# Kernel optimization log

Measured on AMD Instinct MI355X. Metric: run time of the kernel, lower is better.

## Reference

```python
import jax, jax.numpy as jnp
import numpy as np
from functools import partial

B, C, COND, L_MEL, HOP, UP = 4, 32, 80, 2048, 8, 8
LAYERS, K, HID, KPK, EMB = 4, 3, 64, 3, 512
L_AUD = L_MEL * UP  # 16384


def conv1d(x, w, b=None, padding=0, dilation=1):
    # x: (B, Cin, L), w: (Cout, Cin, K) -- PyTorch Conv1d semantics
    out = jax.lax.conv_general_dilated(
        x, w, window_strides=(1,), padding=[(padding, padding)],
        rhs_dilation=(dilation,), dimension_numbers=('NCH', 'OIH', 'NCH'))
    if b is not None:
        out = out + b[None, :, None]
    return out


def conv_transpose1d(x, w, stride, pad):
    # PyTorch ConvTranspose1d, weight (Cin, Cout, K), no bias, output_padding=0
    k = w.shape[-1]
    w_eq = jnp.flip(w, -1).transpose(1, 0, 2)  # (Cout, Cin, K)
    lo = k - 1 - pad
    return jax.lax.conv_general_dilated(
        x, w_eq, window_strides=(1,), padding=[(lo, lo)],
        lhs_dilation=(stride,), dimension_numbers=('NCH', 'OIH', 'NCH'))


def lrelu(x, s):
    return jnp.where(x >= 0, x, s * x)


def kernel_predictor(cond, kp_in_w, kp_in_b, kp_res_w1, kp_res_b1,
                     kp_res_w2, kp_res_b2, kp_k_w, kp_k_b, kp_b_w, kp_b_b):
    # FastDiff/UnivNet KernelPredictor: input conv (k=5) + 3 residual blocks + heads
    h = lrelu(conv1d(cond, kp_in_w, kp_in_b, padding=2), 0.1)
    for i in range(3):  # fixed small structural loop
        r = lrelu(conv1d(h, kp_res_w1[i], kp_res_b1[i], padding=1), 0.1)
        r = lrelu(conv1d(r, kp_res_w2[i], kp_res_b2[i], padding=1), 0.1)
        h = h + r
    bsz, _, ln = cond.shape
    k = conv1d(h, kp_k_w, kp_k_b, padding=1)
    b = conv1d(h, kp_b_w, kp_b_b, padding=1)
    kernels = k.reshape(bsz, LAYERS, C, 2 * C, K, ln)
    bias = b.reshape(bsz, LAYERS, 2 * C, ln)
    return kernels, bias


def location_variable_convolution(x, kernel, bias, dilation, hop):
    # x: (B, Cin, L), kernel: (B, Cin, Cout, K, Lf), bias: (B, Cout, Lf)
    bsz, cin, ln = x.shape
    _, _, cout, ks, lf = kernel.shape
    pad = dilation * (ks - 1) // 2
    xp = jnp.pad(x, ((0, 0), (0, 0), (pad, pad)))
    # gather per-frame sliding windows: (Lf, hop, K)
    pos = (jnp.arange(lf) * hop)[:, None, None] \
        + jnp.arange(hop)[None, :, None] \
        + (jnp.arange(ks) * dilation)[None, None, :]
    xw = xp[:, :, pos]  # (B, Cin, Lf, hop, K)
    o = jnp.einsum('bilsk,biokl->bols', xw, kernel)  # (B, Cout, Lf, hop)
    o = o + bias[:, :, :, None]
    return o.reshape(bsz, cout, lf * hop)


def forward(x, audio_down, c, noise_embedding, fc_t_w, fc_t_b, up_w, conv_w,
            kp_in_w, kp_in_b, kp_res_w1, kp_res_b1, kp_res_w2, kp_res_b2,
            kp_k_w, kp_k_b, kp_b_w, kp_b_b):
    noise = (noise_embedding @ fc_t_w.T + fc_t_b)[:, :, None]  # (B, 80, 1)
    condition = c + noise
    kernels, bias = kernel_predictor(condition, kp_in_w, kp_in_b, kp_res_w1,
                                     kp_res_b1, kp_res_w2, kp_res_b2,
                                     kp_k_w, kp_k_b, kp_b_w, kp_b_b)
    h = lrelu(x, 0.2)
    h = conv_transpose1d(h, up_w, UP, UP // 2)  # (B, 32, 16384)
    for i in range(LAYERS):
        h = h + audio_down
        y = lrelu(h, 0.2)
        y = conv1d(y, conv_w[i], padding=3 ** i, dilation=3 ** i)
        y = lrelu(y, 0.2)
        y = location_variable_convolution(y, kernels[:, i], bias[:, i], 1, HOP)
        h = h + jax.nn.sigmoid(y[:, :C, :]) * jnp.tanh(y[:, C:, :])
    return h


def setup_inputs() -> dict:
    key = jax.random.key(0)
    ks = jax.random.split(key, 20)
    s = 0.02
    kch = LAYERS * C * (2 * C) * K  # 24576
    bch = LAYERS * 2 * C            # 256
    return {
        'x': jax.random.normal(ks[0], (B, C, L_MEL), jnp.float32),
        'audio_down': jax.random.normal(ks[1], (B, C, L_AUD), jnp.float32),
        'c': jax.random.normal(ks[2], (B, COND, L_MEL), jnp.float32),
        'noise_embedding': jax.random.normal(ks[3], (B, EMB), jnp.float32),
        'fc_t_w': jax.random.normal(ks[4], (COND, EMB), jnp.float32) * s,
        'fc_t_b': jnp.zeros((COND,), jnp.float32),
        'up_w': jax.random.normal(ks[5], (C, C, UP * 2), jnp.float32) * s,
        'conv_w': jax.random.normal(ks[6], (LAYERS, C, C, K), jnp.float32) * s,
        'kp_in_w': jax.random.normal(ks[7], (HID, COND, 5), jnp.float32) * s,
        'kp_in_b': jnp.zeros((HID,), jnp.float32),
        'kp_res_w1': jax.random.normal(ks[8], (3, HID, HID, KPK), jnp.float32) * s,
        'kp_res_b1': jnp.zeros((3, HID), jnp.float32),
        'kp_res_w2': jax.random.normal(ks[9], (3, HID, HID, KPK), jnp.float32) * s,
        'kp_res_b2': jnp.zeros((3, HID), jnp.float32),
        'kp_k_w': jax.random.normal(ks[10], (kch, HID, KPK), jnp.float32) * s,
        'kp_k_b': jnp.zeros((kch,), jnp.float32),
        'kp_b_w': jax.random.normal(ks[11], (bch, HID, KPK), jnp.float32) * s,
        'kp_b_b': jnp.zeros((bch,), jnp.float32),
    }


def reference(x, audio_down, c, noise_embedding, fc_t_w, fc_t_b, up_w, conv_w,
              kp_in_w, kp_in_b, kp_res_w1, kp_res_b1, kp_res_w2, kp_res_b2,
              kp_k_w, kp_k_b, kp_b_w, kp_b_b):
    return forward(x, audio_down, c, noise_embedding, fc_t_w, fc_t_b, up_w,
                   conv_w, kp_in_w, kp_in_b, kp_res_w1, kp_res_b1, kp_res_w2,
                   kp_res_b2, kp_k_w, kp_k_b, kp_b_w, kp_b_b)
```

## Files before the change

kernel.cpp:

```cpp
#include <hip/hip_runtime.h>
#include <math.h>

#define B_      4
#define C_      32
#define COND_   80
#define LMEL_   2048
#define HOP_    8
#define UP_     8
#define LAYERS_ 4
#define K_      3
#define HID_    64
#define KPK_    3
#define EMB_    512
#define LAUD_   (LMEL_*UP_)
#define KCH_    (LAYERS_*C_*2*C_*K_)
#define BCH_    (LAYERS_*2*C_)
#define Y2S     (LAUD_ + 8)

typedef short v8s __attribute__((ext_vector_type(8)));
typedef float v4f __attribute__((ext_vector_type(4)));

__device__ __forceinline__ float lrelu_(float v, float s) { return v >= 0.f ? v : s * v; }

__device__ __forceinline__ unsigned short f2bf(float f) {
  unsigned int x = __float_as_uint(f);
  unsigned int r = (x + 0x7FFFu + ((x >> 16) & 1u)) >> 16;
  return (unsigned short)r;
}

#define GLOAD16(GSRC, LDST)                                              \
  __builtin_amdgcn_global_load_lds(                                     \
      (const __attribute__((address_space(1))) unsigned int*)(GSRC),    \
      (__attribute__((address_space(3))) unsigned int*)(LDST), 16, 0, 0)

__global__ void k_mkWTs(const float* __restrict__ src, float* __restrict__ dst,
                        int S, int OC, int ICK) {
  int idx = blockIdx.x*256 + threadIdx.x;
  if (idx >= S*OC*ICK) return;
  int s = idx / (OC*ICK), rem = idx % (OC*ICK);
  int oc = rem / ICK, ick = rem % ICK;
  dst[s*OC*ICK + ick*OC + oc] = src[idx];
}

__global__ void k_noise_cond(const float* __restrict__ ne, const float* __restrict__ fw,
                             const float* __restrict__ fb, const float* __restrict__ c,
                             float* __restrict__ cond) {
  int b = blockIdx.x / COND_;
  int cc = blockIdx.x % COND_;
  __shared__ float red[256];
  float p = 0.f;
  for (int j = threadIdx.x; j < EMB_; j += 256)
    p += ne[b*EMB_ + j] * fw[cc*EMB_ + j];
  red[threadIdx.x] = p;
  __syncthreads();
  for (int s = 128; s > 0; s >>= 1) {
    if (threadIdx.x < s) red[threadIdx.x] += red[threadIdx.x + s];
    __syncthreads();
  }
  float noise = red[0] + fb[cc];
  const float* cp = c + (b*COND_ + cc)*LMEL_;
  float* op = cond + (b*COND_ + cc)*LMEL_;
  for (int l = threadIdx.x; l < LMEL_; l += 256) op[l] = cp[l] + noise;
}

__global__ __launch_bounds__(256) void k_kp_in(const float* __restrict__ cond, const float* __restrict__ wT,
                                               const float* __restrict__ bias, float* __restrict__ out) {
  const int T = 32;
  int b  = blockIdx.x / (LMEL_/T);
  int lb = (blockIdx.x % (LMEL_/T)) * T;
  __shared__ float sc[COND_][T + 4];
  for (int idx = threadIdx.x; idx < COND_*(T+4); idx += 256) {
    int cc = idx / (T+4), j = idx % (T+4);
    int l = lb + j - 2;
    sc[cc][j] = (l >= 0 && l < LMEL_) ? cond[(b*COND_ + cc)*LMEL_ + l] : 0.f;
  }
  __syncthreads();
  int ch = threadIdx.x & 63;
  int lq = threadIdx.x >> 6;
  float acc[8];
#pragma unroll
  for (int ii = 0; ii < 8; ii++) acc[ii] = bias[ch];
  for (int cc = 0; cc < COND_; cc++) {
    float r[12];
#pragma unroll
    for (int j = 0; j < 12; j++) r[j] = sc[cc][lq*8 + j];
#pragma unroll
    for (int k = 0; k < 5; k++) {
      float wv = wT[(cc*5 + k)*64 + ch];
#pragma unroll
      for (int ii = 0; ii < 8; ii++) acc[ii] = fmaf(wv, r[ii + k], acc[ii]);
    }
  }
  float* op = out + (b*HID_ + ch)*LMEL_ + lb + lq*8;
#pragma unroll
  for (int ii = 0; ii < 8; ii++) acc[ii] = lrelu_(acc[ii], 0.1f);
  *reinterpret_cast<float4*>(&op[0]) = make_float4(acc[0], acc[1], acc[2], acc[3]);
  *reinterpret_cast<float4*>(&op[4]) = make_float4(acc[4], acc[5], acc[6], acc[7]);
}

__global__ __launch_bounds__(256) void k_kp_res2(const float* __restrict__ in,
                                                 const float* __restrict__ w1T, const float* __restrict__ b1,
                                                 const float* __restrict__ w2T, const float* __restrict__ b2,
                                                 float* __restrict__ out) {
  const int T = 32;
  int b  = blockIdx.x / (LMEL_/T);
  int lb = (blockIdx.x % (LMEL_/T)) * T;
  __shared__ float si[HID_][38];
  __shared__ float sr[HID_][38];
  for (int idx = threadIdx.x; idx < HID_*36; idx += 256) {
    int cc = idx / 36, j = idx % 36;
    int l = lb - 2 + j;
    si[cc][j] = (l >= 0 && l < LMEL_) ? in[(b*HID_ + cc)*LMEL_ + l] : 0.f;
  }
  __syncthreads();
  int ch = threadIdx.x & 63;
  int lq = threadIdx.x >> 6;
  {
    float b1v = b1[ch];
    float a1[9];
#pragma unroll
    for (int jj = 0; jj < 9; jj++) a1[jj] = b1v;
    for (int cc = 0; cc < HID_; cc++) {
      float r[11];
#pragma unroll
      for (int j = 0; j < 11; j++) r[j] = si[cc][lq*9 + j];
#pragma unroll
      for (int k = 0; k < 3; k++) {
        float wv = w1T[(cc*3 + k)*64 + ch];
#pragma unroll
        for (int jj = 0; jj < 9; jj++) a1[jj] = fmaf(wv, r[jj + k], a1[jj]);
      }
    }
#pragma unroll
    for (int jj = 0; jj < 9; jj++) {
      int m = lq*9 + jj;
      if (m < 34) sr[ch][m] = lrelu_(a1[jj], 0.1f);
    }
  }
  __syncthreads();
  {
    float b2v = b2[ch];
    float a2[8];
#pragma unroll
    for (int jj = 0; jj < 8; jj++) a2[jj] = b2v;
    for (int cc = 0; cc < HID_; cc++) {
      float r[10];
#pragma unroll
      for (int j = 0; j < 10; j++) r[j] = sr[cc][lq*8 + j];
#pragma unroll
      for (int k = 0; k < 3; k++) {
        float wv = w2T[(cc*3 + k)*64 + ch];
#pragma unroll
        for (int jj = 0; jj < 8; jj++) a2[jj] = fmaf(wv, r[jj + k], a2[jj]);
      }
    }
    float* op = out + (b*HID_ + ch)*LMEL_ + lb + lq*8;
    float v[8];
#pragma unroll
    for (int jj = 0; jj < 8; jj++)
      v[jj] = si[ch][lq*8 + jj + 2] + lrelu_(a2[jj], 0.1f);
    *reinterpret_cast<float4*>(&op[0]) = make_float4(v[0], v[1], v[2], v[3]);
    *reinterpret_cast<float4*>(&op[4]) = make_float4(v[4], v[5], v[6], v[7]);
  }
}

__global__ __launch_bounds__(256) void k_kp_bias(const float* __restrict__ in, const float* __restrict__ wT,
                                                 const float* __restrict__ bias, float* __restrict__ out) {
  const int T = 16;
  int b  = blockIdx.x / (LMEL_/T);
  int lb = (blockIdx.x % (LMEL_/T)) * T;
  __shared__ float si[HID_][T + 2];
  for (int idx = threadIdx.x; idx < HID_*(T+2); idx += 256) {
    int cc = idx / (T+2), j = idx % (T+2);
    int l = lb + j - 1;
    si[cc][j] = (l >= 0 && l < LMEL_) ? in[(b*HID_ + cc)*LMEL_ + l] : 0.f;
  }
  __syncthreads();
  int ch = threadIdx.x;
  float acc[T];
  float bv = bias[ch];
#pragma unroll
  for (int ii = 0; ii < T; ii++) acc[ii] = bv;
  for (int cc = 0; cc < HID_; cc++) {
    float w0 = wT[(cc*3 + 0)*256 + ch];
    float w1 = wT[(cc*3 + 1)*256 + ch];
    float w2 = wT[(cc*3 + 2)*256 + ch];
#pragma unroll
    for (int ii = 0; ii < T; ii++)
      acc[ii] = fmaf(w0, si[cc][ii], fmaf(w1, si[cc][ii+1], fmaf(w2, si[cc][ii+2], acc[ii])));
  }
  float* op = out + (b*BCH_ + ch)*LMEL_ + lb;
#pragma unroll
  for (int q = 0; q < 4; q++)
    *reinterpret_cast<float4*>(&op[q*4]) = make_float4(acc[q*4], acc[q*4+1], acc[q*4+2], acc[q*4+3]);
}

__global__ void k_mkUp(const float* __restrict__ upw, float* __restrict__ wt) {
  int idx = blockIdx.x*256 + threadIdx.x;
  if (idx >= C_*C_*16) return;
  int co = idx & 31, j = (idx >> 5) & 15, ci = idx >> 9;
  wt[idx] = upw[(ci*C_ + co)*16 + j];
}

#define UT 32
__global__ __launch_bounds__(256) void k_upsample(const float* __restrict__ x, const float* __restrict__ wt,
                                                  float* __restrict__ h) {
  int b  = blockIdx.x / 65;
  int s0 = (blockIdx.x % 65) * UT;
  __shared__ float sw[16384];
  __shared__ float sx[C_][33 + 3];
  for (int idx = threadIdx.x*4; idx < 16384; idx += 1024)
    *reinterpret_cast<float4*>(&sw[idx]) = *reinterpret_cast<const float4*>(&wt[idx]);
  for (int idx = threadIdx.x; idx < C_*33; idx += 256) {
    int ci = idx / 33, i = idx % 33;
    int s = s0 - 1 + i;
    float v = (s >= 0 && s < LMEL_) ? x[(b*C_ + ci)*LMEL_ + s] : 0.f;
    sx[ci][i] = lrelu_(v, 0.2f);
  }
  __syncthreads();
  int co = threadIdx.x & 31, sq = threadIdx.x >> 5;
  float acc[4][8];
#pragma unroll
  for (int k = 0; k < 4; k++)
#pragma unroll
    for (int r = 0; r < 8; r++) acc[k][r] = 0.f;
  for (int ci = 0; ci < C_; ci++) {
    float xv[5];
#pragma unroll
    for (int m = 0; m < 5; m++) xv[m] = sx[ci][sq*4 + m];
    const float* wl = &sw[ci*512 + co];
#pragma unroll
    for (int r = 0; r < 8; r++) {
      float wa = wl[r*32];
      float wb = wl[(r+8)*32];
#pragma unroll
      for (int k = 0; k < 4; k++)
        acc[k][r] = fmaf(wa, xv[k+1], fmaf(wb, xv[k], acc[k][r]));
    }
  }
  float* op = h + ((size_t)b*C_ + co)*LAUD_;
#pragma unroll
  for (int k = 0; k < 4; k++) {
    int s1 = s0 + sq*4 + k;
    int lo = 8*s1 - 4;
    if (lo >= 0 && lo + 4 <= LAUD_)
      *reinterpret_cast<float4*>(&op[lo]) = make_float4(acc[k][0], acc[k][1], acc[k][2], acc[k][3]);
    if (lo >= -4 && lo + 8 <= LAUD_)
      *reinterpret_cast<float4*>(&op[lo+4]) = make_float4(acc[k][4], acc[k][5], acc[k][6], acc[k][7]);
  }
}

__global__ void k_mkA(const float* __restrict__ kw, unsigned short* __restrict__ waf) {
  int idx = blockIdx.x*256 + threadIdx.x;
  if (idx >= KCH_*HID_*KPK_) return;
  int i    = idx & 7;
  int lane = (idx >> 3) & 63;
  int ks   = (idx >> 9) % 6;
  int tile = (idx / 3072) & 3;
  int rk   = idx / 12288;
  int layer = rk / 96, rem = rk % 96, ci = rem / 3, kk = rem % 3;
  int cout = tile*16 + (lane & 15);
  int j    = ks*32 + ((lane >> 4) << 3) + i;
  int row  = ((layer*32 + ci)*64 + cout)*3 + kk;
  waf[idx] = f2bf(kw[row*192 + j]);
}

__global__ void k_mkKbT(const float* __restrict__ kb, float* __restrict__ kbt) {
  int idx = blockIdx.x*256 + threadIdx.x;
  if (idx >= KCH_) return;
  int cr = idx & 15, tile = (idx >> 4) & 3, rk = idx >> 6;
  int layer = rk / 96, rem = rk % 96, ci = rem / 3, kk = rem % 3;
  int cout = tile*16 + cr;
  kbt[idx] = kb[((layer*32 + ci)*64 + cout)*3 + kk];
}

template<int DIL>
__global__ __launch_bounds__(256) void k_dilconv(const float* __restrict__ h, const float* __restrict__ ad,
                                                 const float* __restrict__ wT, float* __restrict__ y2p) {
  const int T = 128;
  int b  = blockIdx.x / (LAUD_/T);
  int tb = (blockIdx.x % (LAUD_/T)) * T;
  const int W = T + 2*DIL;
  __shared__ float ss[C_][T + 2*27 + 4];
  for (int idx = threadIdx.x; idx < C_*W; idx += 256) {
    int ci = idx / W, j = idx % W;
    int t = tb - DIL + j;
    float v = 0.f;
    if (t >= 0 && t < LAUD_) {
      int g = (b*C_ + ci)*LAUD_ + t;
      v = h[g] + ad[g];
    }
    ss[ci][j] = lrelu_(v, 0.2f);
  }
  if (tb == 0 && threadIdx.x < 128) {
    int ci = threadIdx.x >> 2, q = threadIdx.x & 3;
    y2p[(size_t)(b*C_ + ci)*Y2S + q] = 0.f;
  }
  if (tb == LAUD_ - T && threadIdx.x < 128) {
    int ci = threadIdx.x >> 2, q = threadIdx.x & 3;
    y2p[(size_t)(b*C_ + ci)*Y2S + 4 + LAUD_ + q] = 0.f;
  }
  __syncthreads();
  int co = threadIdx.x & 31, tq = threadIdx.x >> 5;
  float acc[16];
#pragma unroll
  for (int ii = 0; ii < 16; ii++) acc[ii] = 0.f;
  for (int ci = 0; ci < C_; ci++) {
    float w0 = wT[(ci*3 + 0)*32 + co];
    float w1 = wT[(ci*3 + 1)*32 + co];
    float w2 = wT[(ci*3 + 2)*32 + co];
#pragma unroll
    for (int ii = 0; ii < 16; ii++) {
      int tl = tq*16 + ii;
      acc[ii] = fmaf(w0, ss[ci][tl], fmaf(w1, ss[ci][tl + DIL], fmaf(w2, ss[ci][tl + 2*DIL], acc[ii])));
    }
  }
  float* op = y2p + (size_t)(b*C_ + co)*Y2S + 4 + tb + tq*16;
#pragma unroll
  for (int ii = 0; ii < 16; ii++) acc[ii] = lrelu_(acc[ii], 0.2f);
#pragma unroll
  for (int q = 0; q < 4; q++)
    *reinterpret_cast<float4*>(&op[q*4]) = make_float4(acc[q*4], acc[q*4+1], acc[q*4+2], acc[q*4+3]);
}

#define NST 96
#define LOADY(SYR, TBASE)                                                        \
  {                                                                              \
    const float* yp = yr + (TBASE);                                              \
    float4 qa = *reinterpret_cast<const float4*>(yp - 4);                        \
    float4 qb = *reinterpret_cast<const float4*>(yp);                            \
    float4 qc = *reinterpret_cast<const float4*>(yp + 4);                        \
    float4 qd = *reinterpret_cast<const float4*>(yp + 8);                        \
    SYR[0] = qa.w;                                                               \
    SYR[1] = qb.x; SYR[2] = qb.y; SYR[3] = qb.z; SYR[4] = qb.w;                  \
    SYR[5] = qc.x; SYR[6] = qc.y; SYR[7] = qc.z; SYR[8] = qc.w;                  \
    SYR[9] = qd.x; SYR[10] = qd.y; SYR[11] = qd.z;                               \
  }

#define STAGE(BOFF, STEP)                                                        \
  {                                                                              \
    int rk4 = (layer*96 + (STEP))*4 + v;                                         \
    const unsigned short* gsrc = waf + (size_t)rk4*3072;                         \
    { int u = tid; int tpx = (u >= 384); int wi = u - tpx*384;                   \
      GLOAD16(gsrc + tpx*6144 + wi*8, (char*)stg + (BOFF) + u*16); }             \
    if (tid < 256) { int u = tid + 512; int wi = u - 384;                        \
      GLOAD16(gsrc + 6144 + wi*8, (char*)stg + (BOFF) + u*16); }                 \
  }

__global__ __launch_bounds__(512, 2) void k_lvc_mfma(
    const float* __restrict__ hkp, const unsigned short* __restrict__ waf,
    const float* __restrict__ kbt, const float* __restrict__ biasb,
    const float* __restrict__ y2p, const float* __restrict__ ad,
    float* __restrict__ h, int layer) {
  int b  = blockIdx.x >> 6;
  int r6 = blockIdx.x & 63;
  int l0 = (r6 >> 1) * 64;
  int v  = r6 & 1;

  __shared__ __align__(16) float pool[14592];
  float* shh = pool;
  unsigned short* FB = (unsigned short*)(pool + 6144);
  float* red = pool + 6144;
  unsigned short* stg = (unsigned short*)pool;

  int tid = threadIdx.x;
  for (int idx = tid; idx < HID_*66; idx += 512) {
    int hh = idx / 66, j = idx % 66;
    int l = l0 - 1 + j;
    shh[hh*66 + j] = (l >= 0 && l < LMEL_) ? hkp[(b*HID_ + hh)*LMEL_ + l] : 0.f;
  }
  __syncthreads();
  for (int u = tid; u < 12288; u += 512) {
    int i = u & 7, lane2 = (u >> 3) & 63, ksf = u >> 9;
    int ks = ksf % 6, fg2 = ksf / 6;
    int k = ks*32 + ((lane2 >> 4) << 3) + i;
    int col = lane2 & 15;
    int hh = k / 3, q = k - hh*3;
    FB[u] = f2bf(shh[hh*66 + fg2*16 + col + q]);
  }
  __syncthreads();

  int wave = tid >> 6, lane = tid & 63;
  int tp = wave & 1, fg = wave >> 1;
  int tile = v + 2*tp;
  int f = lane & 15;

  v8s bfr[6];
#pragma unroll
  for (int ks = 0; ks < 6; ks++)
    bfr[ks] = *reinterpret_cast<const v8s*>(&FB[((fg*6 + ks)*64 + lane)*8]);

  float o[4][8];
#pragma unroll
  for (int r = 0; r < 4; r++)
#pragma unroll
    for (int s = 0; s < 8; s++) o[r][s] = 0.f;

  const float* ybase = y2p + ((size_t)(b*C_))*Y2S + 4;
  const int t0 = (l0 + fg*16 + f)*8;
  const int kbl = ((lane >> 4) << 2);

  STAGE(0, 0)
  __syncthreads();
  int cur = 0, step = 0;

  for (int ci = 0; ci < 32; ci++) {
    const float* yr = ybase + (size_t)ci*Y2S;
    float syr[12];
    LOADY(syr, t0)
#pragma unroll
    for (int kk = 0; kk < 3; kk++) {
      if (step < NST-1) STAGE((cur^1)*12288, step+1)
      const unsigned short* sa = stg + cur*6144 + tp*3072;
      v4f acc = {0.f, 0.f, 0.f, 0.f};
#pragma unroll
      for (int ks = 0; ks < 6; ks++) {
        v8s a = *reinterpret_cast<const v8s*>(sa + ks*512 + lane*8);
        acc = __builtin_amdgcn_mfma_f32_16x16x32_bf16(a, bfr[ks], acc, 0, 0, 0);
      }
      float4 kb4 = *reinterpret_cast<const float4*>(
          kbt + ((layer*96 + step)*4 + tile)*16 + kbl);
#pragma unroll
      for (int r = 0; r < 4; r++) {
        float kern = acc[r] + ((const float*)&kb4)[r];
#pragma unroll
        for (int s = 0; s < 8; s++)
          o[r][s] = fmaf(kern, syr[kk + s], o[r][s]);
      }
      __syncthreads();
      cur ^= 1; step++;
    }
  }

#pragma unroll
  for (int r = 0; r < 4; r++) {
    int cout = tile*16 + kbl + r;
    float bv = biasb[((size_t)b*BCH_ + layer*2*C_ + cout)*LMEL_ + l0 + fg*16 + f];
#pragma unroll
    for (int s = 0; s < 8; s++) o[r][s] += bv;
  }
  if (tp == 1) {
#pragma unroll
    for (int r = 0; r < 4; r++)
#pragma unroll
      for (int s = 0; s < 8; s++)
        red[(fg*64 + lane)*33 + r*8 + s] = o[r][s];
  }
  __syncthreads();
  if (tp == 0) {
#pragma unroll
    for (int r = 0; r < 4; r++) {
      int cout = v*16 + kbl + r;
      size_t base = ((size_t)b*C_ + cout)*LAUD_ + (size_t)(l0 + fg*16 + f)*HOP_;
      float4 h0 = *reinterpret_cast<const float4*>(&h[base]);
      float4 h1 = *reinterpret_cast<const float4*>(&h[base + 4]);
      float4 a0 = *reinterpret_cast<const float4*>(&ad[base]);
      float4 a1 = *reinterpret_cast<const float4*>(&ad[base + 4]);
      float outv[8];
#pragma unroll
      for (int s = 0; s < 8; s++) {
        float vv = o[r][s];
        float tv = red[(fg*64 + lane)*33 + r*8 + s];
        float sig = 1.f / (1.f + __expf(-vv));
        float th  = 1.f - 2.f / (1.f + __expf(2.f*tv));
        float hv = (s < 4) ? ((const float*)&h0)[s] : ((const float*)&h1)[s-4];
        float av = (s < 4) ? ((const float*)&a0)[s] : ((const float*)&a1)[s-4];
        outv[s] = hv + av + sig * th;
      }
      *reinterpret_cast<float4*>(&h[base])     = make_float4(outv[0], outv[1], outv[2], outv[3]);
      *reinterpret_cast<float4*>(&h[base + 4]) = make_float4(outv[4], outv[5], outv[6], outv[7]);
    }
  }
}

extern "C" void kernel_launch(void* const* d_in, const int* in_sizes, int n_in,
                              void* d_out, int out_size, void* d_ws, size_t ws_size,
                              hipStream_t stream) {
  const float* x     = (const float*)d_in[0];
  const float* ad    = (const float*)d_in[1];
  const float* c     = (const float*)d_in[2];
  const float* ne    = (const float*)d_in[3];
  const float* fw    = (const float*)d_in[4];
  const float* fb    = (const float*)d_in[5];
  const float* upw   = (const float*)d_in[6];
  const float* convw = (const float*)d_in[7];
  const float* kinw  = (const float*)d_in[8];
  const float* kinb  = (const float*)d_in[9];
  const float* krw1  = (const float*)d_in[10];
  const float* krb1  = (const float*)d_in[11];
  const float* krw2  = (const float*)d_in[12];
  const float* krb2  = (const float*)d_in[13];
  const float* kkw   = (const float*)d_in[14];
  const float* kkb   = (const float*)d_in[15];
  const float* kbw   = (const float*)d_in[16];
  const float* kbb   = (const float*)d_in[17];
  float* h = (float*)d_out;

  float* ws = (float*)d_ws;
  float* cond   = ws; ws += B_*COND_*LMEL_;
  float* hkpa   = ws; ws += B_*HID_*LMEL_;
  float* hkpb   = ws; ws += B_*HID_*LMEL_;
  float* biasb  = ws; ws += B_*BCH_*LMEL_;
  float* y2p    = ws; ws += B_*C_*Y2S;
  float* kbt    = ws; ws += KCH_;
  float* wtup   = ws; ws += C_*C_*16;
  float* kinwT  = ws; ws += HID_*COND_*5;
  float* krw1T  = ws; ws += 3*HID_*HID_*3;
  float* krw2T  = ws; ws += 3*HID_*HID_*3;
  float* kbwT   = ws; ws += BCH_*HID_*3;
  float* convwT = ws; ws += LAYERS_*C_*C_*3;
  unsigned short* waf = (unsigned short*)ws; ws += (KCH_*HID_*KPK_)/2;

  k_mkA<<<(KCH_*HID_*KPK_ + 255)/256, 256, 0, stream>>>(kkw, waf);
  k_mkKbT<<<(KCH_ + 255)/256, 256, 0, stream>>>(kkb, kbt);
  k_mkUp<<<(C_*C_*16 + 255)/256, 256, 0, stream>>>(upw, wtup);
  k_mkWTs<<<(HID_*COND_*5 + 255)/256, 256, 0, stream>>>(kinw, kinwT, 1, HID_, COND_*5);
  k_mkWTs<<<(3*HID_*HID_*3 + 255)/256, 256, 0, stream>>>(krw1, krw1T, 3, HID_, HID_*3);
  k_mkWTs<<<(3*HID_*HID_*3 + 255)/256, 256, 0, stream>>>(krw2, krw2T, 3, HID_, HID_*3);
  k_mkWTs<<<(BCH_*HID_*3 + 255)/256, 256, 0, stream>>>(kbw, kbwT, 1, BCH_, HID_*3);
  k_mkWTs<<<(LAYERS_*C_*C_*3 + 255)/256, 256, 0, stream>>>(convw, convwT, LAYERS_, C_, C_*3);

  k_noise_cond<<<B_*COND_, 256, 0, stream>>>(ne, fw, fb, c, cond);
  k_kp_in<<<B_*(LMEL_/32), 256, 0, stream>>>(cond, kinwT, kinb, hkpa);
  k_kp_res2<<<B_*(LMEL_/32), 256, 0, stream>>>(hkpa, krw1T + 0*HID_*HID_*3, krb1 + 0*HID_,
                                               krw2T + 0*HID_*HID_*3, krb2 + 0*HID_, hkpb);
  k_kp_res2<<<B_*(LMEL_/32), 256, 0, stream>>>(hkpb, krw1T + 1*HID_*HID_*3, krb1 + 1*HID_,
                                               krw2T + 1*HID_*HID_*3, krb2 + 1*HID_, hkpa);
  k_kp_res2<<<B_*(LMEL_/32), 256, 0, stream>>>(hkpa, krw1T + 2*HID_*HID_*3, krb1 + 2*HID_,
                                               krw2T + 2*HID_*HID_*3, krb2 + 2*HID_, hkpb);
  k_kp_bias<<<B_*(LMEL_/16), 256, 0, stream>>>(hkpb, kbwT, kbb, biasb);
  k_upsample<<<B_*65, 256, 0, stream>>>(x, wtup, h);

  for (int i = 0; i < LAYERS_; i++) {
    const float* wci = convwT + i*C_*C_*3;
    switch (i) {
      case 0: k_dilconv<1 ><<<B_*(LAUD_/128), 256, 0, stream>>>(h, ad, wci, y2p); break;
      case 1: k_dilconv<3 ><<<B_*(LAUD_/128), 256, 0, stream>>>(h, ad, wci, y2p); break;
      case 2: k_dilconv<9 ><<<B_*(LAUD_/128), 256, 0, stream>>>(h, ad, wci, y2p); break;
      case 3: k_dilconv<27><<<B_*(LAUD_/128), 256, 0, stream>>>(h, ad, wci, y2p); break;
    }
    k_lvc_mfma<<<B_*64, 512, 0, stream>>>(hkpb, waf, kbt, biasb, y2p, ad, h, i);
  }
}
```

Before: 534.1 us.

## Deepen LVC weight staging to four buffers and cache inputs in LDS

The LVC MFMA kernel now streams weight tiles through four LDS buffers with a prefetch distance of two steps. It waits with explicit vmcnt counts and raw s_barrier instead of a full __syncthreads per step. The per-block audio window and kernel-bias slices are preloaded into LDS once, so the inner loop no longer issues global loads for them. Shared memory grows from about 58 KB to about 152 KB per block, which likely drops the kernel to one resident block per CU and could cost latency hiding.

New measurement: 502.6 us. 1.06x faster.

```diff
diff --git a/kernel.cpp b/kernel.cpp
--- a/kernel.cpp
+++ b/kernel.cpp
@@ -33,6 +33,8 @@
       (const __attribute__((address_space(1))) unsigned int*)(GSRC),    \
       (__attribute__((address_space(3))) unsigned int*)(LDST), 16, 0, 0)
 
+#define WAITV(N) asm volatile("s_waitcnt vmcnt(" #N ")" ::: "memory")
+
 __global__ void k_mkWTs(const float* __restrict__ src, float* __restrict__ dst,
                         int S, int OC, int ICK) {
   int idx = blockIdx.x*256 + threadIdx.x;
@@ -323,28 +325,14 @@
     *reinterpret_cast<float4*>(&op[q*4]) = make_float4(acc[q*4], acc[q*4+1], acc[q*4+2], acc[q*4+3]);
 }
 
-#define NST 96
-#define LOADY(SYR, TBASE)                                                        \
+#define STAGE(BUF, STEP)                                                         \
   {                                                                              \
-    const float* yp = yr + (TBASE);                                              \
-    float4 qa = *reinterpret_cast<const float4*>(yp - 4);                        \
-    float4 qb = *reinterpret_cast<const float4*>(yp);                            \
-    float4 qc = *reinterpret_cast<const float4*>(yp + 4);                        \
-    float4 qd = *reinterpret_cast<const float4*>(yp + 8);                        \
-    SYR[0] = qa.w;                                                               \
-    SYR[1] = qb.x; SYR[2] = qb.y; SYR[3] = qb.z; SYR[4] = qb.w;                  \
-    SYR[5] = qc.x; SYR[6] = qc.y; SYR[7] = qc.z; SYR[8] = qc.w;                  \
-    SYR[9] = qd.x; SYR[10] = qd.y; SYR[11] = qd.z;                               \
-  }
-
-#define STAGE(BOFF, STEP)                                                        \
-  {                                                                              \
-    int rk4 = (layer*96 + (STEP))*4 + v;                                         \
-    const unsigned short* gsrc = waf + (size_t)rk4*3072;                         \
+    const unsigned short* gsrc = waf + (size_t)((layer*96 + (STEP))*4)*3072;     \
     { int u = tid; int tpx = (u >= 384); int wi = u - tpx*384;                   \
-      GLOAD16(gsrc + tpx*6144 + wi*8, (char*)stg + (BOFF) + u*16); }             \
+      GLOAD16(gsrc + (v + 2*tpx)*3072 + wi*8,                                    \
+              (char*)stg + (BUF)*12288 + u*16); }                                \
     if (tid < 256) { int u = tid + 512; int wi = u - 384;                        \
-      GLOAD16(gsrc + 6144 + wi*8, (char*)stg + (BOFF) + u*16); }                 \
+      GLOAD16(gsrc + (v + 2)*3072 + wi*8, (char*)stg + (BUF)*12288 + u*16); }    \
   }
 
 __global__ __launch_bounds__(512, 2) void k_lvc_mfma(
@@ -357,13 +345,26 @@
   int l0 = (r6 >> 1) * 64;
   int v  = r6 & 1;
 
-  __shared__ __align__(16) float pool[14592];
-  float* shh = pool;
-  unsigned short* FB = (unsigned short*)(pool + 6144);
-  float* red = pool + 6144;
-  unsigned short* stg = (unsigned short*)pool;
+  __shared__ __align__(16) char pool[152064];
+  unsigned short* stg   = (unsigned short*)pool;
+  unsigned short* FB    = (unsigned short*)(pool + 49152);
+  float*          kbt_s = (float*)(pool + 73728);
+  float*          sy    = (float*)(pool + 86016);
+  float*          shh   = (float*)pool;
+  float*          red   = (float*)pool;
 
   int tid = threadIdx.x;
+  {
+    const float* ysrc = y2p + (size_t)(b*C_)*Y2S + 4 + (size_t)l0*8 - 1;
+    for (int idx = tid; idx < 32*514; idx += 512) {
+      int ci = idx / 514, j = idx % 514;
+      sy[ci*516 + j] = ysrc[(size_t)ci*Y2S + j];
+    }
+  }
+  for (int u = tid; u < 3072; u += 512) {
+    int step = u >> 5, tp2 = (u >> 4) & 1, cr = u & 15;
+    kbt_s[u] = kbt[((layer*96 + step)*4 + v + 2*tp2)*16 + cr];
+  }
   for (int idx = tid; idx < HID_*66; idx += 512) {
     int hh = idx / 66, j = idx % 66;
     int l = l0 - 1 + j;
@@ -382,8 +383,8 @@
 
   int wave = tid >> 6, lane = tid & 63;
   int tp = wave & 1, fg = wave >> 1;
-  int tile = v + 2*tp;
   int f = lane & 15;
+  const int kbl = ((lane >> 4) << 2);
 
   v8s bfr[6];
 #pragma unroll
@@ -396,30 +397,43 @@
 #pragma unroll
     for (int s = 0; s < 8; s++) o[r][s] = 0.f;
 
-  const float* ybase = y2p + ((size_t)(b*C_))*Y2S + 4;
-  const int t0 = (l0 + fg*16 + f)*8;
-  const int kbl = ((lane >> 4) << 2);
-
   STAGE(0, 0)
-  __syncthreads();
-  int cur = 0, step = 0;
+  STAGE(1, 1)
+  if (wave < 4) { WAITV(2); } else { WAITV(1); }
+  __builtin_amdgcn_s_barrier();
+
+  const int sybase = (fg*16 + f)*8;
 
   for (int ci = 0; ci < 32; ci++) {
-    const float* yr = ybase + (size_t)ci*Y2S;
     float syr[12];
-    LOADY(syr, t0)
+    {
+      const float* yrow = sy + ci*516 + sybase;
+      float4 q0 = *reinterpret_cast<const float4*>(yrow);
+      float4 q1 = *reinterpret_cast<const float4*>(yrow + 4);
+      float4 q2 = *reinterpret_cast<const float4*>(yrow + 8);
+      syr[0]=q0.x; syr[1]=q0.y; syr[2]=q0.z; syr[3]=q0.w;
+      syr[4]=q1.x; syr[5]=q1.y; syr[6]=q1.z; syr[7]=q1.w;
+      syr[8]=q2.x; syr[9]=q2.y; syr[10]=q2.z; syr[11]=q2.w;
+    }
 #pragma unroll
     for (int kk = 0; kk < 3; kk++) {
-      if (step < NST-1) STAGE((cur^1)*12288, step+1)
-      const unsigned short* sa = stg + cur*6144 + tp*3072;
+      int step = ci*3 + kk;
+      if (step < 94) {
+        STAGE((step + 2) & 3, step + 2)
+        if (wave < 4) { WAITV(2); } else { WAITV(1); }
+      } else {
+        WAITV(0);
+      }
+      __builtin_amdgcn_s_barrier();
+
+      const unsigned short* sa = stg + (step & 3)*6144 + tp*3072;
       v4f acc = {0.f, 0.f, 0.f, 0.f};
 #pragma unroll
       for (int ks = 0; ks < 6; ks++) {
         v8s a = *reinterpret_cast<const v8s*>(sa + ks*512 + lane*8);
         acc = __builtin_amdgcn_mfma_f32_16x16x32_bf16(a, bfr[ks], acc, 0, 0, 0);
       }
-      float4 kb4 = *reinterpret_cast<const float4*>(
-          kbt + ((layer*96 + step)*4 + tile)*16 + kbl);
+      float4 kb4 = *reinterpret_cast<const float4*>(&kbt_s[(step*2 + tp)*16 + kbl]);
 #pragma unroll
       for (int r = 0; r < 4; r++) {
         float kern = acc[r] + ((const float*)&kb4)[r];
@@ -427,14 +441,12 @@
         for (int s = 0; s < 8; s++)
           o[r][s] = fmaf(kern, syr[kk + s], o[r][s]);
       }
-      __syncthreads();
-      cur ^= 1; step++;
     }
   }
 
 #pragma unroll
   for (int r = 0; r < 4; r++) {
-    int cout = tile*16 + kbl + r;
+    int cout = (v + 2*tp)*16 + kbl + r;
     float bv = biasb[((size_t)b*BCH_ + layer*2*C_ + cout)*LMEL_ + l0 + fg*16 + f];
 #pragma unroll
     for (int s = 0; s < 8; s++) o[r][s] += bv;
```
